# Optimization experiments

Hardware: AMD Instinct MI355X
Metric: run time of the kernel (lower is better)

The kernel has to match this reference:

```python
import jax, jax.numpy as jnp
import numpy as np

B, T, K, H = 2, 2048, 1024, 16


def setup_inputs() -> dict:
    key = jax.random.key(0)
    ks = jax.random.split(key, 9)
    sc = 0.02
    return {
        "x": jax.random.normal(ks[0], (B, T, K), dtype=jnp.float32),
        "Wq_w": jax.random.normal(ks[1], (K, K), dtype=jnp.float32) * sc,
        "Wq_b": jax.random.normal(ks[2], (K,), dtype=jnp.float32) * sc,
        "Wk_w": jax.random.normal(ks[3], (K, K), dtype=jnp.float32) * sc,
        "Wk_b": jax.random.normal(ks[4], (K,), dtype=jnp.float32) * sc,
        "Wv_w": jax.random.normal(ks[5], (K, K), dtype=jnp.float32) * sc,
        "Wv_b": jax.random.normal(ks[6], (K,), dtype=jnp.float32) * sc,
        "Wo_w": jax.random.normal(ks[7], (K, K), dtype=jnp.float32) * sc,
        "Wo_b": jax.random.normal(ks[8], (K,), dtype=jnp.float32) * sc,
    }


def reference(x, Wq_w, Wq_b, Wk_w, Wk_b, Wv_w, Wv_b, Wo_w, Wo_b):
    b, t, k = x.shape
    h = H
    s = k // h
    # nn.Linear: y = x @ W^T + b
    q = x @ Wq_w.T + Wq_b
    kk = x @ Wk_w.T + Wk_b
    v = x @ Wv_w.T + Wv_b
    # [b, t, h, s] -> [b, h, t, s]
    q = q.reshape(b, t, h, s).transpose(0, 2, 1, 3)
    kk = kk.reshape(b, t, h, s).transpose(0, 2, 1, 3)
    v = v.reshape(b, t, h, s).transpose(0, 2, 1, 3)
    # scores [b, h, t, t]
    dot = jnp.einsum("bhqd,bhkd->bhqk", q, kk)
    # causal mask: upper triangle (offset=1) set to -inf BEFORE scaling
    causal = jnp.tril(jnp.ones((t, t), dtype=bool))
    dot = jnp.where(causal, dot, -jnp.inf)
    # NOTE: original scales by sqrt(k) (full model dim), not sqrt(head_dim)
    dot = dot / jnp.sqrt(jnp.asarray(k, dot.dtype))
    attn = jax.nn.softmax(dot, axis=-1)
    out = jnp.einsum("bhqk,bhkd->bhqd", attn, v)  # [b, h, t, s]
    out = out.transpose(0, 2, 1, 3).reshape(b, t, k)
    return out @ Wo_w.T + Wo_b
```

## Files before the change

kernel.cpp:

```cpp
#include <hip/hip_runtime.h>

typedef unsigned short u16;
typedef unsigned int u32;
typedef __bf16 bf16x8 __attribute__((ext_vector_type(8)));
typedef float f32x4 __attribute__((ext_vector_type(4)));
typedef unsigned short u16x8 __attribute__((ext_vector_type(8)));
typedef unsigned int u32x4 __attribute__((ext_vector_type(4)));

#define B_ 2
#define T_ 2048
#define K_ 1024
#define H_ 16
#define S_ 64
#define MKC 4194304
#define QSCALE 0.04508422f

__device__ __forceinline__ u16 f2bf(float f) {
  unsigned int u = __builtin_bit_cast(unsigned int, f);
  u += 0x7fffu + ((u >> 16) & 1u);
  return (u16)(u >> 16);
}

__device__ __forceinline__ f32x4 MFMA(bf16x8 a, bf16x8 b, f32x4 c) {
  return __builtin_amdgcn_mfma_f32_16x16x32_bf16(a, b, c, 0, 0, 0);
}

__device__ __forceinline__ void gld16(const void* g, void* l) {
  __builtin_amdgcn_global_load_lds((const __attribute__((address_space(1))) void*)g,
                                   (__attribute__((address_space(3))) void*)l, 16, 0, 0);
}

template <int N>
__device__ __forceinline__ void waitv() {
  asm volatile("s_waitcnt vmcnt(%0)" ::"i"(N) : "memory");
}
__device__ __forceinline__ void memfence_barrier() {
  asm volatile("" ::: "memory");
  __builtin_amdgcn_s_barrier();
}

__global__ __launch_bounds__(256) void cvt_all(const float* __restrict__ x,
                                               const float* __restrict__ W0,
                                               const float* __restrict__ W1,
                                               const float* __restrict__ W2,
                                               const float* __restrict__ W3,
                                               u16* __restrict__ xb,
                                               u16* __restrict__ wb) {
  const int i = blockIdx.x * 256 + threadIdx.x;
  const float* src;
  u16* dst;
  if (i < 524288) {
    src = x + (size_t)i * 8;
    dst = xb + (size_t)i * 8;
  } else {
    const int j = i - 524288;
    const int sel = j >> 17;
    const float* W = sel == 0 ? W0 : sel == 1 ? W1 : sel == 2 ? W2 : W3;
    src = W + (size_t)(j & 131071) * 8;
    dst = wb + (size_t)j * 8;
  }
  const float4* s = (const float4*)src;
  float4 f0 = s[0], f1 = s[1];
  u16x8 p;
  p[0] = f2bf(f0.x); p[1] = f2bf(f0.y); p[2] = f2bf(f0.z); p[3] = f2bf(f0.w);
  p[4] = f2bf(f1.x); p[5] = f2bf(f1.y); p[6] = f2bf(f1.z); p[7] = f2bf(f1.w);
  *(u16x8*)dst = p;
}

template <int OMODE, int BM, int BN>
__global__ __launch_bounds__(256) void gemm16(const u16* __restrict__ A,
                                              const u16* __restrict__ Bm,
                                              const float* __restrict__ b0,
                                              const float* __restrict__ b1,
                                              const float* __restrict__ b2,
                                              void* __restrict__ C0,
                                              int M, int N, int K) {
  constexpr int MF = BM / 32;
  constexpr int NF = BN / 32;
  constexpr int SOPS = BM / 64 + BN / 64;
  __shared__ u16 As[2][BM * 32];
  __shared__ u16 Bs[2][BN * 32];
  const int bm = blockIdx.x * BM;
  const int bn = blockIdx.y * BN;
  const int tid = threadIdx.x;
  const int w = tid >> 6, lane = tid & 63;
  const int wr = (w >> 1) * (BM / 2), wc = (w & 1) * (BN / 2);
  const int lr = lane & 15, g = lane >> 4;
  const int lk = (g ^ ((lr >> 1) & 3)) * 8;
  const int srow = lane >> 2;
  const int scol = ((lane & 3) ^ ((lane >> 3) & 3)) * 8;

  f32x4 acc[MF][NF] = {};

  auto stg = [&](int buf, int k0) {
#pragma unroll
    for (int i = 0; i < BM / 64; ++i) {
      const int rbase = (i * 4 + w) * 16;
      gld16(A + (size_t)(bm + rbase + srow) * K + k0 + scol, &As[buf][rbase * 32]);
    }
#pragma unroll
    for (int i = 0; i < BN / 64; ++i) {
      const int rbase = (i * 4 + w) * 16;
      gld16(Bm + (size_t)(bn + rbase + srow) * K + k0 + scol, &Bs[buf][rbase * 32]);
    }
  };

  stg(0, 0);
  const int NK = K >> 5;
  for (int kk = 0; kk < NK; ++kk) {
    const int buf = kk & 1;
    const bool pf = (kk + 1 < NK);
    if (pf) {
      stg(buf ^ 1, (kk + 1) * 32);
      waitv<SOPS>();
    } else {
      waitv<0>();
    }
    __builtin_amdgcn_s_barrier();
    bf16x8 af[MF], bfr[NF];
#pragma unroll
    for (int m = 0; m < MF; ++m)
      af[m] = *(const bf16x8*)&As[buf][(wr + m * 16 + lr) * 32 + lk];
#pragma unroll
    for (int n = 0; n < NF; ++n)
      bfr[n] = *(const bf16x8*)&Bs[buf][(wc + n * 16 + lr) * 32 + lk];
#pragma unroll
    for (int m = 0; m < MF; ++m)
#pragma unroll
      for (int n = 0; n < NF; ++n)
        acc[m][n] = MFMA(af[m], bfr[n], acc[m][n]);
    memfence_barrier();
  }

  const int sel = (OMODE == 2) ? 0 : (bn >> 10);
  const float* bp = (OMODE == 2) ? b0 : (sel == 0 ? b0 : sel == 1 ? b1 : b2);
#pragma unroll
  for (int n = 0; n < NF; ++n) {
    const int col = bn + wc + n * 16 + lr;
    const float bv = bp[(OMODE == 2) ? col : (col & 1023)];
#pragma unroll
    for (int m = 0; m < MF; ++m) {
#pragma unroll
      for (int r = 0; r < 4; ++r) {
        const int row = bm + wr + m * 16 + g * 4 + r;
        float v = acc[m][n][r] + bv;
        if (OMODE == 2) {
          ((float*)C0)[(size_t)row * N + col] = v;
        } else {
          u16* dst = (u16*)C0;
          const int cc = col & 1023;
          if (sel == 2) {
            const int bb = row >> 11, t = row & 2047, hh = cc >> 6, ss = cc & 63;
            dst[(size_t)2 * MKC + (((size_t)(bb * H_ + hh) * S_ + ss) << 11) + t] = f2bf(v);
          } else {
            if (sel == 0) v *= QSCALE;
            dst[(size_t)sel * MKC + (size_t)row * 1024 + cc] = f2bf(v);
          }
        }
      }
    }
  }
}

__global__ __launch_bounds__(256) void attn_fwd(const u16* __restrict__ Q,
                                                const u16* __restrict__ Kb,
                                                const u16* __restrict__ Vt,
                                                u16* __restrict__ O) {
  __shared__ u16 Ks[2][64 * 64];
  __shared__ u16 Vs[2][64 * 64];
  const int tid = threadIdx.x;
  const int w = tid >> 6, lane = tid & 63;
  const int qh = lane & 15;
  const int g = lane >> 4;
  const int bh = blockIdx.x;
  const int b = bh >> 4, h = bh & 15;
  const int yy = blockIdx.y;

  const int srow = lane >> 3;
  const int sl8 = ((lane & 7) ^ srow) * 8;
  int kvp[2];
#pragma unroll
  for (int i = 0; i < 2; ++i) {
    const int rho = w * 16 + i * 8 + srow;
    const int a = rho >> 4;
    kvp[i] = ((a >> 1) << 5) | (((rho >> 2) & 3) << 3) | ((a & 1) << 2) | (rho & 3);
  }
  const int ksw = qh & 7;
  u16x8 ov;
#pragma unroll
  for (int i = 0; i < 8; ++i) ov[i] = 0x3F80;
  const bf16x8 ones = __builtin_bit_cast(bf16x8, ov);

  for (int seg = 0; seg < 2; ++seg) {
    const int qtile = seg ? (31 - yy) : yy;
    const int qb = qtile * 64;
    const int qw = qb + w * 16;
    const int myq = qw + qh;
    const int nk = qtile + 1;

    const size_t qoff = (size_t)(b * T_ + qw + qh) * K_ + h * S_ + g * 8;
    const bf16x8 bq0 = *(const bf16x8*)(Q + qoff);
    const bf16x8 bq1 = *(const bf16x8*)(Q + qoff + 32);

    const u16* kq0 = Kb + (size_t)(b * T_ + kvp[0]) * K_ + h * S_ + sl8;
    const u16* kq1 = Kb + (size_t)(b * T_ + kvp[1]) * K_ + h * S_ + sl8;
    const u16* vq0 = Vt + (size_t)(bh * S_ + w * 16 + srow) * T_ + sl8;
    const u16* vq1 = Vt + (size_t)(bh * S_ + w * 16 + 8 + srow) * T_ + sl8;

    auto stageK = [&](int buf) {
      gld16(kq0, &Ks[buf][(w * 16) * 64]);
      gld16(kq1, &Ks[buf][(w * 16 + 8) * 64]);
      kq0 += 64 * K_; kq1 += 64 * K_;
    };
    auto stageV = [&](int buf) {
      gld16(vq0, &Vs[buf][(w * 16) * 64]);
      gld16(vq1, &Vs[buf][(w * 16 + 8) * 64]);
      vq0 += 64; vq1 += 64;
    };

    f32x4 o[4] = {};
    f32x4 o_l = {};
    f32x4 sA[4], sB[4];

    auto QKT = [&](int buf, f32x4 (&sO)[4]) {
      __builtin_amdgcn_s_setprio(1);
#pragma unroll
      for (int a = 0; a < 4; ++a) {
        const u16* kr = &Ks[buf][(a * 16 + qh) * 64];
        const bf16x8 kf0 = *(const bf16x8*)(kr + ((g ^ ksw) * 8));
        const bf16x8 kf1 = *(const bf16x8*)(kr + (((4 + g) ^ ksw) * 8));
        f32x4 z = {0.f, 0.f, 0.f, 0.f};
        z = MFMA(kf0, bq0, z);
        sO[a] = MFMA(kf1, bq1, z);
      }
      __builtin_amdgcn_s_setprio(0);
    };

    auto SMPV = [&](f32x4 (&sIn)[4], int buf, int k0) {
      float p[4][4];
      if (k0 + 63 > qw) {
        const int thr = myq - k0 - (g << 3);
#pragma unroll
        for (int a = 0; a < 4; ++a)
#pragma unroll
          for (int r = 0; r < 4; ++r) {
            const int C = ((a >> 1) << 5) + ((a & 1) << 2) + r;
            p[a][r] = (C <= thr) ? __builtin_amdgcn_exp2f(sIn[a][r]) : 0.f;
          }
      } else {
#pragma unroll
        for (int a = 0; a < 4; ++a)
#pragma unroll
          for (int r = 0; r < 4; ++r)
            p[a][r] = __builtin_amdgcn_exp2f(sIn[a][r]);
      }

      __builtin_amdgcn_s_setprio(1);
#pragma unroll
      for (int c = 0; c < 2; ++c) {
        u32 t0, t1, t2, t3;
        asm("v_cvt_pk_bf16_f32 %0, %1, %2" : "=v"(t0) : "v"(p[2 * c][0]), "v"(p[2 * c][1]));
        asm("v_cvt_pk_bf16_f32 %0, %1, %2" : "=v"(t1) : "v"(p[2 * c][2]), "v"(p[2 * c][3]));
        asm("v_cvt_pk_bf16_f32 %0, %1, %2" : "=v"(t2) : "v"(p[2 * c + 1][0]), "v"(p[2 * c + 1][1]));
        asm("v_cvt_pk_bf16_f32 %0, %1, %2" : "=v"(t3) : "v"(p[2 * c + 1][2]), "v"(p[2 * c + 1][3]));
        u32x4 tv; tv[0] = t0; tv[1] = t1; tv[2] = t2; tv[3] = t3;
        const bf16x8 pa = __builtin_bit_cast(bf16x8, tv);
        o_l = MFMA(pa, ones, o_l);
#pragma unroll
        for (int nn = 0; nn < 4; ++nn) {
          const bf16x8 vf =
              *(const bf16x8*)(&Vs[buf][(16 * nn + qh) * 64] + (((c * 4 + g) ^ ksw) * 8));
          o[nn] = MFMA(pa, vf, o[nn]);
        }
      }
      __builtin_amdgcn_s_setprio(0);
    };

    stageK(0); stageV(0);
    waitv<0>();
    __builtin_amdgcn_s_barrier();
    QKT(0, sA);
    if (nk > 1) { stageK(1); stageV(1); }

    int kt = 0;
    for (;;) {
      {
        const bool hn = kt + 1 < nk;
        if (hn) waitv<2>(); else waitv<0>();
        __builtin_amdgcn_s_barrier();
        if (hn) { QKT(1, sB); if (kt + 2 < nk) stageK(0); }
        SMPV(sA, 0, kt * 64);
        memfence_barrier();
        if (kt + 2 < nk) stageV(0);
        if (!hn) break;
        ++kt;
      }
      {
        const bool hn = kt + 1 < nk;
        if (hn) waitv<2>(); else waitv<0>();
        __builtin_amdgcn_s_barrier();
        if (hn) { QKT(0, sA); if (kt + 2 < nk) stageK(1); }
        SMPV(sB, 1, kt * 64);
        memfence_barrier();
        if (kt + 2 < nk) stageV(1);
        if (!hn) break;
        ++kt;
      }
    }

#pragma unroll
    for (int r = 0; r < 4; ++r) {
      const float inv = 1.f / o_l[r];
      const size_t row = (size_t)(b * T_ + qw + 4 * g + r);
#pragma unroll
      for (int nn = 0; nn < 4; ++nn)
        O[row * K_ + h * S_ + nn * 16 + qh] = f2bf(o[nn][r] * inv);
    }
  }
}

extern "C" void kernel_launch(void* const* d_in, const int* in_sizes, int n_in,
                              void* d_out, int out_size, void* d_ws, size_t ws_size,
                              hipStream_t stream) {
  (void)in_sizes; (void)n_in; (void)out_size; (void)ws_size;
  const float* x  = (const float*)d_in[0];
  const float* Wq = (const float*)d_in[1];
  const float* bq = (const float*)d_in[2];
  const float* Wk = (const float*)d_in[3];
  const float* bk = (const float*)d_in[4];
  const float* Wv = (const float*)d_in[5];
  const float* bv = (const float*)d_in[6];
  const float* Wo = (const float*)d_in[7];
  const float* bo = (const float*)d_in[8];
  float* out = (float*)d_out;

  const size_t MK = (size_t)MKC;
  const size_t WK = (size_t)K_ * K_;
  u16* Qb  = (u16*)d_ws;
  u16* Kbf = Qb + MK;
  u16* Vtb = Kbf + MK;
  u16* AO  = Vtb + MK;
  u16* xb  = AO + MK;
  u16* Wqkv = xb + MK;
  u16* Wob  = Wqkv + 3 * WK;

  dim3 blk(256);
  cvt_all<<<dim3(4096), blk, 0, stream>>>(x, Wq, Wk, Wv, Wo, xb, Wqkv);
  gemm16<3, 64, 128><<<dim3(64, 24), blk, 0, stream>>>(xb, Wqkv, bq, bk, bv, Qb,
                                                       B_ * T_, 3 * K_, K_);
  attn_fwd<<<dim3(B_ * H_, 16), blk, 0, stream>>>(Qb, Kbf, Vtb, AO);
  gemm16<2, 64, 64><<<dim3(64, 16), blk, 0, stream>>>(AO, Wob, bo, bo, bo, out,
                                                      B_ * T_, K_, K_);
}
```

Baseline: 120.2 us.

## Deepen LDS pipelines in GEMM and attention, enlarge GEMM tiles

The GEMM moves from double to triple buffering and issues the prefetch two k-steps ahead, right after the barrier. That drops the second barrier per iteration. Attention gets a 4-deep K/V ring, stages K and V together three tiles ahead, and removes the mid-iteration barrier. GEMM tiles grow to 128 rows, which halves the grid for both projections. Together these aim to hide more global-load latency and cut barrier count. The cost is more LDS per block, possibly lower occupancy, and fewer blocks to fill the CUs.

```diff
diff --git a/kernel.cpp b/kernel.cpp
--- a/kernel.cpp
+++ b/kernel.cpp
@@ -33,10 +33,6 @@
 template <int N>
 __device__ __forceinline__ void waitv() {
   asm volatile("s_waitcnt vmcnt(%0)" ::"i"(N) : "memory");
-}
-__device__ __forceinline__ void memfence_barrier() {
-  asm volatile("" ::: "memory");
-  __builtin_amdgcn_s_barrier();
 }
 
 __global__ __launch_bounds__(256) void cvt_all(const float* __restrict__ x,
@@ -78,8 +74,8 @@
   constexpr int MF = BM / 32;
   constexpr int NF = BN / 32;
   constexpr int SOPS = BM / 64 + BN / 64;
-  __shared__ u16 As[2][BM * 32];
-  __shared__ u16 Bs[2][BN * 32];
+  __shared__ u16 As[3][BM * 32];
+  __shared__ u16 Bs[3][BN * 32];
   const int bm = blockIdx.x * BM;
   const int bn = blockIdx.y * BN;
   const int tid = threadIdx.x;
@@ -106,30 +102,27 @@
   };
 
   stg(0, 0);
+  stg(1, 32);
   const int NK = K >> 5;
+  int rb = 0, sb = 2;
   for (int kk = 0; kk < NK; ++kk) {
-    const int buf = kk & 1;
-    const bool pf = (kk + 1 < NK);
-    if (pf) {
-      stg(buf ^ 1, (kk + 1) * 32);
-      waitv<SOPS>();
-    } else {
-      waitv<0>();
-    }
+    if (kk + 1 < NK) waitv<SOPS>(); else waitv<0>();
     __builtin_amdgcn_s_barrier();
+    if (kk + 2 < NK) stg(sb, (kk + 2) * 32);
     bf16x8 af[MF], bfr[NF];
 #pragma unroll
     for (int m = 0; m < MF; ++m)
-      af[m] = *(const bf16x8*)&As[buf][(wr + m * 16 + lr) * 32 + lk];
+      af[m] = *(const bf16x8*)&As[rb][(wr + m * 16 + lr) * 32 + lk];
 #pragma unroll
     for (int n = 0; n < NF; ++n)
-      bfr[n] = *(const bf16x8*)&Bs[buf][(wc + n * 16 + lr) * 32 + lk];
+      bfr[n] = *(const bf16x8*)&Bs[rb][(wc + n * 16 + lr) * 32 + lk];
 #pragma unroll
     for (int m = 0; m < MF; ++m)
 #pragma unroll
       for (int n = 0; n < NF; ++n)
         acc[m][n] = MFMA(af[m], bfr[n], acc[m][n]);
-    memfence_barrier();
+    rb = (rb + 1 == 3) ? 0 : rb + 1;
+    sb = (sb + 1 == 3) ? 0 : sb + 1;
   }
 
   const int sel = (OMODE == 2) ? 0 : (bn >> 10);
@@ -166,8 +159,8 @@
                                                 const u16* __restrict__ Kb,
                                                 const u16* __restrict__ Vt,
                                                 u16* __restrict__ O) {
-  __shared__ u16 Ks[2][64 * 64];
-  __shared__ u16 Vs[2][64 * 64];
+  __shared__ u16 Ks[4][64 * 64];
+  __shared__ u16 Vs[4][64 * 64];
   const int tid = threadIdx.x;
   const int w = tid >> 6, lane = tid & 63;
   const int qh = lane & 15;
@@ -207,15 +200,12 @@
     const u16* vq0 = Vt + (size_t)(bh * S_ + w * 16 + srow) * T_ + sl8;
     const u16* vq1 = Vt + (size_t)(bh * S_ + w * 16 + 8 + srow) * T_ + sl8;
 
-    auto stageK = [&](int buf) {
+    auto stage = [&](int buf) {
       gld16(kq0, &Ks[buf][(w * 16) * 64]);
       gld16(kq1, &Ks[buf][(w * 16 + 8) * 64]);
-      kq0 += 64 * K_; kq1 += 64 * K_;
-    };
-    auto stageV = [&](int buf) {
       gld16(vq0, &Vs[buf][(w * 16) * 64]);
       gld16(vq1, &Vs[buf][(w * 16 + 8) * 64]);
-      vq0 += 64; vq1 += 64;
+      kq0 += 64 * K_; kq1 += 64 * K_; vq0 += 64; vq1 += 64;
     };
 
     f32x4 o[4] = {};
@@ -276,33 +266,34 @@
       __builtin_amdgcn_s_setprio(0);
     };
 
-    stageK(0); stageV(0);
-    waitv<0>();
+    stage(0);
+    if (nk > 1) stage(1);
+    if (nk > 2) stage(2);
+    if (nk > 2) waitv<8>();
+    else if (nk > 1) waitv<4>();
+    else waitv<0>();
     __builtin_amdgcn_s_barrier();
     QKT(0, sA);
-    if (nk > 1) { stageK(1); stageV(1); }
 
     int kt = 0;
     for (;;) {
       {
         const bool hn = kt + 1 < nk;
-        if (hn) waitv<2>(); else waitv<0>();
+        if (kt + 2 < nk) waitv<4>(); else waitv<0>();
         __builtin_amdgcn_s_barrier();
-        if (hn) { QKT(1, sB); if (kt + 2 < nk) stageK(0); }
-        SMPV(sA, 0, kt * 64);
-        memfence_barrier();
-        if (kt + 2 < nk) stageV(0);
+        if (kt + 3 < nk) stage((kt + 3) & 3);
+        if (hn) QKT((kt + 1) & 3, sB);
+        SMPV(sA, kt & 3, kt * 64);
         if (!hn) break;
         ++kt;
       }
       {
         const bool hn = kt + 1 < nk;
-        if (hn) waitv<2>(); else waitv<0>();
+        if (kt + 2 < nk) waitv<4>(); else waitv<0>();
         __builtin_amdgcn_s_barrier();
-        if (hn) { QKT(0, sA); if (kt + 2 < nk) stageK(1); }
-        SMPV(sB, 1, kt * 64);
-        memfence_barrier();
-        if (kt + 2 < nk) stageV(1);
+        if (kt + 3 < nk) stage((kt + 3) & 3);
+        if (hn) QKT((kt + 1) & 3, sA);
+        SMPV(sB, kt & 3, kt * 64);
         if (!hn) break;
         ++kt;
       }
@@ -346,9 +337,9 @@
 
   dim3 blk(256);
   cvt_all<<<dim3(4096), blk, 0, stream>>>(x, Wq, Wk, Wv, Wo, xb, Wqkv);
-  gemm16<3, 64, 128><<<dim3(64, 24), blk, 0, stream>>>(xb, Wqkv, bq, bk, bv, Qb,
-                                                       B_ * T_, 3 * K_, K_);
+  gemm16<3, 128, 128><<<dim3(32, 24), blk, 0, stream>>>(xb, Wqkv, bq, bk, bv, Qb,
+                                                        B_ * T_, 3 * K_, K_);
   attn_fwd<<<dim3(B_ * H_, 16), blk, 0, stream>>>(Qb, Kbf, Vtb, AO);
-  gemm16<2, 64, 64><<<dim3(64, 16), blk, 0, stream>>>(AO, Wob, bo, bo, bo, out,
-                                                      B_ * T_, K_, K_);
-}
+  gemm16<2, 128, 64><<<dim3(32, 16), blk, 0, stream>>>(AO, Wob, bo, bo, bo, out,
+                                                       B_ * T_, K_, K_);
+}
```

Result: faster. 104.5 us (-13.1%).
